# Kernel optimization log

Hardware: AMD Instinct MI355X
Metric: run time of the kernel (lower is better)

## Reference

```python
import jax, jax.numpy as jnp
import numpy as np

NEG_SLOPE = 0.2  # PyG GATConv default leaky_relu slope


def gat_layer(x, src, dst, W, a_src, a_dst, n_nodes, heads, ch):
    # x: [N, in_dim]; W: [in_dim, heads*ch]
    h = (x @ W).reshape(n_nodes, heads, ch)              # [N, H, C]
    e_s = jnp.einsum('nhc,hc->nh', h, a_src)             # [N, H]
    e_d = jnp.einsum('nhc,hc->nh', h, a_dst)             # [N, H]
    e = jax.nn.leaky_relu(e_s[src] + e_d[dst], NEG_SLOPE)  # [E, H]
    # segment softmax over incoming edges of each destination node
    m = jax.lax.stop_gradient(jax.ops.segment_max(e, dst, num_segments=n_nodes))
    w = jnp.exp(e - m[dst])                              # [E, H]
    z = jax.ops.segment_sum(w, dst, num_segments=n_nodes)  # [N, H]
    alpha = w / z[dst]                                   # [E, H]
    msg = h[src] * alpha[:, :, None]                     # [E, H, C]
    out = jax.ops.segment_sum(msg, dst, num_segments=n_nodes)  # [N, H, C]
    return out


def setup_inputs() -> dict:
    key = jax.random.key(0)
    ks = jax.random.split(key, 12)
    N, E, D, H = 50000, 800000, 128, 4
    x = jax.random.normal(ks[0], (N, D), dtype=jnp.float32)
    edge_index = jax.random.randint(ks[1], (2, E), 0, N, dtype=jnp.int64)
    s1 = 1.0 / np.sqrt(D)
    s2 = 1.0 / np.sqrt(D * H)
    W1 = jax.random.normal(ks[2], (D, H * D), dtype=jnp.float32) * s1
    a1_src = jax.random.normal(ks[3], (H, D), dtype=jnp.float32) * s1
    a1_dst = jax.random.normal(ks[4], (H, D), dtype=jnp.float32) * s1
    b1 = jax.random.normal(ks[5], (H * D,), dtype=jnp.float32) * 0.01
    W2 = jax.random.normal(ks[6], (H * D, D), dtype=jnp.float32) * s2
    a2_src = jax.random.normal(ks[7], (1, D), dtype=jnp.float32) * s1
    a2_dst = jax.random.normal(ks[8], (1, D), dtype=jnp.float32) * s1
    b2 = jax.random.normal(ks[9], (D,), dtype=jnp.float32) * 0.01
    fc_w = jax.random.normal(ks[10], (D, 1), dtype=jnp.float32) * s1
    fc_b = jax.random.normal(ks[11], (1,), dtype=jnp.float32) * 0.01
    return {"x": x, "edge_index": edge_index, "W1": W1, "a1_src": a1_src,
            "a1_dst": a1_dst, "b1": b1, "W2": W2, "a2_src": a2_src,
            "a2_dst": a2_dst, "b2": b2, "fc_w": fc_w, "fc_b": fc_b}


def reference(x, edge_index, W1, a1_src, a1_dst, b1, W2, a2_src, a2_dst, b2, fc_w, fc_b):
    N, D = x.shape
    H = a1_src.shape[0]
    # add self-loops (PyG GATConv default add_self_loops=True)
    loop = jnp.arange(N, dtype=edge_index.dtype)
    src = jnp.concatenate([edge_index[0], loop])
    dst = jnp.concatenate([edge_index[1], loop])
    # conv1: heads=4, concat=True -> [N, H*D]
    h1 = gat_layer(x, src, dst, W1, a1_src, a1_dst, N, H, D)
    h1 = jax.nn.relu(h1.reshape(N, H * D) + b1)
    # dropout p=0.2 is identity in eval mode
    # conv2: heads=1 -> [N, D]
    h2 = gat_layer(h1, src, dst, W2, a2_src, a2_dst, N, 1, D)
    h2 = h2.reshape(N, D) + b2
    return h2 @ fc_w + fc_b  # [N, 1]
```

## Files before the change

kernel.cpp:

```cpp
#include <hip/hip_runtime.h>
#include <cstdint>
#include <cstddef>

constexpr int kN   = 50000;
constexpr int kE   = 800000;
constexpr int kEt  = kE + kN;
constexpr float kSlope = 0.2f;
constexpr int kScanB = (kN + 255) / 256;
constexpr int kConvB = (kN * 16 + 255) / 256;
constexpr int kHistB = (kEt + 255) / 256;
constexpr int kQuarB = (kN * 16 + 255) / 256;
constexpr int kHChunks = 64;
constexpr int kChunk   = (kEt + kHChunks - 1) / kHChunks;
constexpr int kHRanges = 4;
constexpr int kRangeN  = kN / kHRanges;
constexpr int kRangeH  = kRangeN / 2;
constexpr int kHalfN   = kN / 2;

typedef __attribute__((ext_vector_type(8))) short bf8_t;
typedef __attribute__((ext_vector_type(4))) float f4_t;
typedef __attribute__((ext_vector_type(2))) float f2_t;

__device__ __align__(16) unsigned short g_xb[(size_t)kN * 128];
__device__ __align__(16) unsigned short g_aggx[(size_t)kN * 512];
__device__ __align__(16) unsigned short g_w1t[4 * 128 * 128];
__device__ __align__(16) float g_u[3][512];
__device__ __align__(16) float g_es1[kN * 4];
__device__ __align__(16) float g_ed1[kN * 4];
__device__ __align__(16) float2 g_sp[kN];
__device__ float g_ed2[kN];
__device__ float g_c0;
__device__ __align__(16) float g_p1s[4 * 128];
__device__ __align__(16) float g_p1d[4 * 128];
__device__ int g_deg[kN];
__device__ int g_ptr[kN + 1];
__device__ int g_rank[kEt];
__device__ __align__(16) unsigned g_bhist[(size_t)kHChunks * kHalfN];
__device__ __align__(16) unsigned g_bbase[(size_t)kHChunks * kHalfN];
__device__ int g_srcs[kEt];
__device__ int g_bsum[kScanB];

__device__ __forceinline__ float lrelu(float x) { return x > 0.f ? x : kSlope * x; }

__device__ __forceinline__ bf8_t bf8_zero() {
  uint4 z = make_uint4(0u, 0u, 0u, 0u);
  return *(bf8_t*)&z;
}

__device__ __forceinline__ unsigned short f2bf1(float v) {
  unsigned u = __float_as_uint(v);
  unsigned r = (u + 0x7FFFu + ((u >> 16) & 1u)) >> 16;
  return (unsigned short)r;
}

__global__ __launch_bounds__(256) void k_hist(const int* __restrict__ ei) {
  __shared__ unsigned sh[kRangeH];
  const int b = blockIdx.x, t = threadIdx.x;
  const int chunk = b & (kHChunks - 1);
  const int rr = b >> 6;
  const int lo = rr * kRangeN, hi = lo + kRangeN;
  for (int i = t; i < kRangeH; i += 256) sh[i] = 0u;
  __syncthreads();
  const int beg = chunk * kChunk, end = min(beg + kChunk, kEt);
  for (int e = beg + t; e < end; e += 256) {
    int d = (e < kE) ? ei[kE + e] : e - kE;
    if (d >= lo && d < hi) {
      unsigned inc = (d & 1) ? 0x10000u : 1u;
      unsigned old = atomicAdd(&sh[(d - lo) >> 1], inc);
      g_rank[e] = (d & 1) ? (int)(old >> 16) : (int)(old & 0xFFFFu);
    }
  }
  __syncthreads();
  unsigned* dst = g_bhist + (size_t)chunk * kHalfN + rr * kRangeH;
  for (int i = t; i < kRangeH; i += 256) dst[i] = sh[i];
}

__global__ __launch_bounds__(256) void k_pass2() {
  const int i = blockIdx.x * 256 + threadIdx.x;
  if (i >= kHalfN) return;
  unsigned c0 = 0, c1 = 0;
#pragma unroll 4
  for (int b = 0; b < kHChunks; ++b) {
    unsigned v = g_bhist[(size_t)b * kHalfN + i];
    g_bbase[(size_t)b * kHalfN + i] = c0 | (c1 << 16);
    c0 += v & 0xFFFFu;
    c1 += v >> 16;
  }
  *(int2*)&g_deg[2 * i] = make_int2((int)c0, (int)c1);
}

__global__ __launch_bounds__(256) void k_init(const float* __restrict__ x,
    const float* __restrict__ W1, const float* __restrict__ W2,
    const float* __restrict__ a1s, const float* __restrict__ a1d,
    const float* __restrict__ a2s, const float* __restrict__ a2d,
    const float* __restrict__ b2, const float* __restrict__ fcw,
    const float* __restrict__ fcb) {
  const int b = blockIdx.x, t = threadIdx.x;
  if (b < 197) {
    int i = b * 256 + t;
    if (i < kN) {
      g_sp[i] = make_float2(0.f, 0.f);
      g_ed2[i] = 0.f;
    }
  } else if (b < 453) {
    int gid = (b - 197) * 256 + t;
    int h = gid >> 14, rem = gid & 16383;
    int c = rem >> 7, j = rem & 127;
    float v = W1[(size_t)c * 512 + h * 128 + j];
    g_w1t[((size_t)h * 128 + j) * 128 + c] = f2bf1(v);
  } else if (b < 457) {
    int gid = (b - 453) * 256 + t;
    int which = gid >> 9, idx = gid & 511;
    int h = idx >> 7, k = idx & 127;
    const float* a = which ? a1d : a1s;
    const float* wrow = W1 + (size_t)k * 512 + h * 128;
    float s = 0.f;
#pragma unroll 8
    for (int c = 0; c < 128; ++c) s += wrow[c] * a[h * 128 + c];
    (which ? g_p1d : g_p1s)[idx] = s;
  } else if (b < 463) {
    int gid = (b - 457) * 256 + t;
    if (gid < 1536) {
      int v = gid >> 9, k = gid & 511;
      const float* vv = v == 0 ? a2s : v == 1 ? a2d : fcw;
      const float* wrow = W2 + (size_t)k * 128;
      float s = 0.f;
#pragma unroll 8
      for (int c = 0; c < 128; ++c) s += wrow[c] * vv[c];
      g_u[v][k] = s;
    }
  } else if (b < 464) {
    if (t < 64) {
      float s = b2[t] * fcw[t] + b2[64 + t] * fcw[64 + t];
#pragma unroll
      for (int off = 32; off > 0; off >>= 1) s += __shfl_down(s, off);
      if (t == 0) g_c0 = s + fcb[0];
    }
  } else {
    int g = (b - 464) * 256 + t;
    if (g < kN * 16) {
      const float* xp = x + (size_t)g * 8;
      float4 f0 = *(const float4*)xp;
      float4 f1 = *(const float4*)(xp + 4);
      unsigned w0 = (unsigned)f2bf1(f0.x) | ((unsigned)f2bf1(f0.y) << 16);
      unsigned w1 = (unsigned)f2bf1(f0.z) | ((unsigned)f2bf1(f0.w) << 16);
      unsigned w2 = (unsigned)f2bf1(f1.x) | ((unsigned)f2bf1(f1.y) << 16);
      unsigned w3 = (unsigned)f2bf1(f1.z) | ((unsigned)f2bf1(f1.w) << 16);
      *(uint4*)(g_xb + (size_t)g * 8) = make_uint4(w0, w1, w2, w3);
    }
  }
}

__device__ __forceinline__ void scores1_body(const float* __restrict__ x,
                                             int bid, int t) {
  const int lane = t & 63;
  const int qt = lane >> 4, ql = lane & 15;
  const int n = ((bid * 256 + t) >> 6) * 4 + qt;
  if (n >= kN) return;
  const float* xp = x + (size_t)n * 128 + ql * 8;
  float4 xa = *(const float4*)xp;
  float4 xb = *(const float4*)(xp + 4);
  float s[4], d[4];
#pragma unroll
  for (int h = 0; h < 4; ++h) {
    const float* ps = g_p1s + h * 128 + ql * 8;
    const float* pd = g_p1d + h * 128 + ql * 8;
    s[h] = xa.x * ps[0] + xa.y * ps[1] + xa.z * ps[2] + xa.w * ps[3]
         + xb.x * ps[4] + xb.y * ps[5] + xb.z * ps[6] + xb.w * ps[7];
    d[h] = xa.x * pd[0] + xa.y * pd[1] + xa.z * pd[2] + xa.w * pd[3]
         + xb.x * pd[4] + xb.y * pd[5] + xb.z * pd[6] + xb.w * pd[7];
  }
#pragma unroll
  for (int off = 1; off < 16; off <<= 1) {
#pragma unroll
    for (int h = 0; h < 4; ++h) {
      s[h] += __shfl_xor(s[h], off);
      d[h] += __shfl_xor(d[h], off);
    }
  }
  if (ql == 0) {
    *(float4*)(g_es1 + (size_t)n * 4) = make_float4(s[0], s[1], s[2], s[3]);
    *(float4*)(g_ed1 + (size_t)n * 4) = make_float4(d[0], d[1], d[2], d[3]);
  }
}

__global__ __launch_bounds__(256) void k_scanA(const float* __restrict__ x) {
  __shared__ int s[256];
  const int b = blockIdx.x, t = threadIdx.x;
  if (b >= kScanB) {
    scores1_body(x, b - kScanB, t);
    return;
  }
  const int i = b * 256 + t;
  int d = (i < kN) ? g_deg[i] : 0;
  s[t] = d;
  __syncthreads();
  for (int off = 1; off < 256; off <<= 1) {
    int v = s[t];
    int u = (t >= off) ? s[t - off] : 0;
    __syncthreads();
    s[t] = v + u;
    __syncthreads();
  }
  if (t == 255) g_bsum[b] = s[255];
  if (i < kN) g_ptr[i] = s[t] - d;
}

__global__ __launch_bounds__(256) void k_scanC() {
  __shared__ int s[256];
  const int b = blockIdx.x, t = threadIdx.x;
  int v = (t < kScanB) ? g_bsum[t] : 0;
  s[t] = v;
  __syncthreads();
  for (int off = 1; off < 256; off <<= 1) {
    int a = s[t];
    int u = (t >= off) ? s[t - off] : 0;
    __syncthreads();
    s[t] = a + u;
    __syncthreads();
  }
  const int boff = (b > 0) ? s[b - 1] : 0;
  __syncthreads();
  const int i = b * 256 + t;
  if (i < kN) g_ptr[i] = g_ptr[i] + boff;
  if (b == 0 && t == 0) g_ptr[kN] = kEt;
}

__global__ __launch_bounds__(256) void k_scatter(const int* __restrict__ ei) {
  int e = blockIdx.x * 256 + threadIdx.x;
  if (e >= kEt) return;
  int s, d;
  if (e < kE) { s = ei[e]; d = ei[kE + e]; } else { s = d = e - kE; }
  const int b = e / kChunk;
  unsigned base = g_bbase[(size_t)b * kHalfN + (d >> 1)];
  base = (d & 1) ? (base >> 16) : (base & 0xFFFFu);
  g_srcs[g_ptr[d] + (int)base + g_rank[e]] = s;
}

__global__ __launch_bounds__(256) void k_agg1x() {
  const int lane = threadIdx.x & 63;
  const int qt = lane >> 4, ql = lane & 15;
  const int n = ((blockIdx.x * 256 + threadIdx.x) >> 6) * 4 + qt;
  if (n >= kN) return;
  const int beg = g_ptr[n], end = g_ptr[n + 1];
  const float4 ed = *(const float4*)(g_ed1 + (size_t)n * 4);
  const int lbase = qt * 16;
  float z0 = 0.f, z1 = 0.f, z2 = 0.f, z3 = 0.f;
  f2_t acc[4][4] = {};
  for (int base = beg; base < end; base += 16) {
    const int cnt = min(16, end - base);
    int s = 0;
    float w0 = 0.f, w1 = 0.f, w2 = 0.f, w3 = 0.f;
    if (ql < cnt) {
      s = g_srcs[base + ql];
      float4 es = *(const float4*)(g_es1 + (size_t)s * 4);
      w0 = __expf(lrelu(es.x + ed.x));
      w1 = __expf(lrelu(es.y + ed.y));
      w2 = __expf(lrelu(es.z + ed.z));
      w3 = __expf(lrelu(es.w + ed.w));
      z0 += w0; z1 += w1; z2 += w2; z3 += w3;
    }
    auto proc = [&](const uint4& uu, int e) {
      float b0 = __shfl(w0, lbase + e), b1 = __shfl(w1, lbase + e);
      float b2 = __shfl(w2, lbase + e), b3 = __shfl(w3, lbase + e);
      f2_t bb0 = b0, bb1 = b1, bb2 = b2, bb3 = b3;
      unsigned ws[4] = {uu.x, uu.y, uu.z, uu.w};
#pragma unroll
      for (int d = 0; d < 4; ++d) {
        f2_t fv;
        fv[0] = __uint_as_float(ws[d] << 16);
        fv[1] = __uint_as_float(ws[d] & 0xFFFF0000u);
        acc[0][d] += bb0 * fv;
        acc[1][d] += bb1 * fv;
        acc[2][d] += bb2 * fv;
        acc[3][d] += bb3 * fv;
      }
    };
    int e = 0;
    for (; e + 4 <= cnt; e += 4) {
      int sj0 = __shfl(s, lbase + e);
      int sj1 = __shfl(s, lbase + e + 1);
      int sj2 = __shfl(s, lbase + e + 2);
      int sj3 = __shfl(s, lbase + e + 3);
      uint4 u0 = *(const uint4*)(g_xb + (size_t)sj0 * 128 + ql * 8);
      uint4 u1 = *(const uint4*)(g_xb + (size_t)sj1 * 128 + ql * 8);
      uint4 u2 = *(const uint4*)(g_xb + (size_t)sj2 * 128 + ql * 8);
      uint4 u3 = *(const uint4*)(g_xb + (size_t)sj3 * 128 + ql * 8);
      proc(u0, e);
      proc(u1, e + 1);
      proc(u2, e + 2);
      proc(u3, e + 3);
    }
    for (; e < cnt; ++e) {
      int sj = __shfl(s, lbase + e);
      uint4 uu = *(const uint4*)(g_xb + (size_t)sj * 128 + ql * 8);
      proc(uu, e);
    }
  }
#pragma unroll
  for (int off = 1; off < 16; off <<= 1) {
    z0 += __shfl_xor(z0, off); z1 += __shfl_xor(z1, off);
    z2 += __shfl_xor(z2, off); z3 += __shfl_xor(z3, off);
  }
  const float iz[4] = {1.f / z0, 1.f / z1, 1.f / z2, 1.f / z3};
  const size_t nb = (size_t)n * 512 + ql * 8;
#pragma unroll
  for (int h = 0; h < 4; ++h) {
    unsigned wd[4];
#pragma unroll
    for (int d = 0; d < 4; ++d) {
      f2_t v = acc[h][d] * iz[h];
      wd[d] = (unsigned)f2bf1(v[0]) | ((unsigned)f2bf1(v[1]) << 16);
    }
    *(uint4*)(g_aggx + nb + h * 128) = make_uint4(wd[0], wd[1], wd[2], wd[3]);
  }
}

__global__ __launch_bounds__(256) void k_fused(const float* __restrict__ b1) {
  __shared__ float sred[2][64][3];
  const int t = threadIdx.x;
  const int lane = t & 63, w = t >> 6;
  const int wrow = w >> 1, wcol = w & 1;
  const int ln15 = lane & 15, q = lane >> 4, qo = q * 8;
  const int row0 = blockIdx.y * 64;
  const int h = blockIdx.z;

  float part[2][4][3] = {};
  f4_t h1acc[2][4] = {};
#pragma unroll
  for (int ks = 0; ks < 128; ks += 32) {
    bf8_t ah[2];
#pragma unroll
    for (int i = 0; i < 2; ++i) {
      int r = row0 + wrow * 32 + i * 16 + ln15;
      ah[i] = bf8_zero();
      if (r < kN)
        ah[i] = *(const bf8_t*)&g_aggx[(size_t)r * 512 + h * 128 + ks + qo];
    }
#pragma unroll
    for (int j = 0; j < 4; ++j) {
      size_t gb = ((size_t)h * 128 + wcol * 64 + j * 16 + ln15) * 128 + ks + qo;
      bf8_t bh = *(const bf8_t*)&g_w1t[gb];
#pragma unroll
      for (int i = 0; i < 2; ++i)
        h1acc[i][j] = __builtin_amdgcn_mfma_f32_16x16x32_bf16(ah[i], bh, h1acc[i][j], 0, 0, 0);
    }
  }
#pragma unroll
  for (int j = 0; j < 4; ++j) {
    int col = h * 128 + wcol * 64 + j * 16 + ln15;
    float bv = b1[col];
    float u0 = g_u[0][col], u1 = g_u[1][col], u2 = g_u[2][col];
#pragma unroll
    for (int i = 0; i < 2; ++i)
#pragma unroll
      for (int reg = 0; reg < 4; ++reg) {
        float v = fmaxf(h1acc[i][j][reg] + bv, 0.f);
        part[i][reg][0] += v * u0;
        part[i][reg][1] += v * u1;
        part[i][reg][2] += v * u2;
      }
  }
#pragma unroll
  for (int off = 1; off < 16; off <<= 1)
#pragma unroll
    for (int i = 0; i < 2; ++i)
#pragma unroll
      for (int reg = 0; reg < 4; ++reg)
#pragma unroll
        for (int v = 0; v < 3; ++v)
          part[i][reg][v] += __shfl_xor(part[i][reg][v], off);
  if (ln15 == 0) {
#pragma unroll
    for (int i = 0; i < 2; ++i)
#pragma unroll
      for (int reg = 0; reg < 4; ++reg) {
        int rl = wrow * 32 + i * 16 + q * 4 + reg;
#pragma unroll
        for (int v = 0; v < 3; ++v) sred[wcol][rl][v] = part[i][reg][v];
      }
  }
  __syncthreads();
  if (t < 192) {
    int row = t / 3, v = t - row * 3;
    float s = sred[0][row][v] + sred[1][row][v];
    int r = row0 + row;
    if (r < kN) {
      float* dst = v == 0 ? &g_sp[r].x : v == 1 ? &g_ed2[r] : &g_sp[r].y;
      atomicAdd(dst, s);
    }
  }
}

__global__ __launch_bounds__(256) void k_agg2s(float* __restrict__ out) {
  const int lane = threadIdx.x & 63;
  const int qt = lane >> 4, ql = lane & 15;
  const int n = ((blockIdx.x * 256 + threadIdx.x) >> 6) * 4 + qt;
  if (n >= kN) return;
  const int beg = g_ptr[n], end = g_ptr[n + 1];
  const float ed = g_ed2[n];
  float zp = 0.f, num = 0.f;
  for (int slot = beg + ql; slot < end; slot += 16) {
    int s = g_srcs[slot];
    float2 sp = g_sp[s];
    float w = __expf(lrelu(sp.x + ed));
    zp += w;
    num += w * sp.y;
  }
#pragma unroll
  for (int off = 1; off < 16; off <<= 1) {
    zp  += __shfl_xor(zp, off);
    num += __shfl_xor(num, off);
  }
  if (ql == 0) out[n] = num / zp + g_c0;
}

extern "C" void kernel_launch(void* const* d_in, const int* in_sizes, int n_in,
                              void* d_out, int out_size, void* d_ws, size_t ws_size,
                              hipStream_t stream) {
  const float* x   = (const float*)d_in[0];
  const int*   ei  = (const int*)d_in[1];
  const float* W1  = (const float*)d_in[2];
  const float* a1s = (const float*)d_in[3];
  const float* a1d = (const float*)d_in[4];
  const float* b1  = (const float*)d_in[5];
  const float* W2  = (const float*)d_in[6];
  const float* a2s = (const float*)d_in[7];
  const float* a2d = (const float*)d_in[8];
  const float* b2  = (const float*)d_in[9];
  const float* fcw = (const float*)d_in[10];
  const float* fcb = (const float*)d_in[11];
  float* out = (float*)d_out;
  (void)d_ws; (void)ws_size; (void)in_sizes; (void)n_in; (void)out_size;

  k_hist<<<kHChunks * kHRanges, 256, 0, stream>>>(ei);
  k_init<<<464 + kConvB, 256, 0, stream>>>(x, W1, W2, a1s, a1d,
                                           a2s, a2d, b2, fcw, fcb);
  k_pass2<<<(kHalfN + 255) / 256, 256, 0, stream>>>();
  k_scanA<<<kScanB + kQuarB, 256, 0, stream>>>(x);
  k_scanC<<<kScanB, 256, 0, stream>>>();
  k_scatter<<<kHistB, 256, 0, stream>>>(ei);

  k_agg1x<<<kQuarB, 256, 0, stream>>>();

  dim3 gf(1, (kN + 63) / 64, 4);
  k_fused<<<gf, 256, 0, stream>>>(b1);

  k_agg2s<<<kQuarB, 256, 0, stream>>>(out);
}
```

Before: 260.6 us.

## Fuse layer-1 aggregation with MFMA projection via shared-memory staging

Merges the layer-1 edge aggregation kernel and the MFMA projection kernel into one kernel. Each block aggregates 32 destination rows into a padded bf16 tile in LDS, then runs the 4-head W1 MFMA and the reductions against the layer-2 vectors directly from LDS. This removes the 50 MB bf16 g_aggx round trip through global memory and one launch. Because each block now owns complete rows, the atomicAdds become plain stores and the zero-initialisation in k_init is dropped. The cost is a 33 KB LDS tile per block, which limits occupancy, a smaller 32-row MFMA tile that reuses each W1 fragment less, and a block-wide barrier between the gather and matmul phases.

Measured after the change: 267.2 us. 1.03x slower.

```diff
diff --git a/kernel.cpp b/kernel.cpp
--- a/kernel.cpp
+++ b/kernel.cpp
@@ -16,13 +16,15 @@
 constexpr int kRangeN  = kN / kHRanges;
 constexpr int kRangeH  = kRangeN / 2;
 constexpr int kHalfN   = kN / 2;
+constexpr int kRows  = 32;
+constexpr int kFB    = (kN + kRows - 1) / kRows;
+constexpr int kPitch = 520;
 
 typedef __attribute__((ext_vector_type(8))) short bf8_t;
 typedef __attribute__((ext_vector_type(4))) float f4_t;
 typedef __attribute__((ext_vector_type(2))) float f2_t;
 
 __device__ __align__(16) unsigned short g_xb[(size_t)kN * 128];
-__device__ __align__(16) unsigned short g_aggx[(size_t)kN * 512];
 __device__ __align__(16) unsigned short g_w1t[4 * 128 * 128];
 __device__ __align__(16) float g_u[3][512];
 __device__ __align__(16) float g_es1[kN * 4];
@@ -42,11 +44,6 @@
 
 __device__ __forceinline__ float lrelu(float x) { return x > 0.f ? x : kSlope * x; }
 
-__device__ __forceinline__ bf8_t bf8_zero() {
-  uint4 z = make_uint4(0u, 0u, 0u, 0u);
-  return *(bf8_t*)&z;
-}
-
 __device__ __forceinline__ unsigned short f2bf1(float v) {
   unsigned u = __float_as_uint(v);
   unsigned r = (u + 0x7FFFu + ((u >> 16) & 1u)) >> 16;
@@ -96,20 +93,14 @@
     const float* __restrict__ b2, const float* __restrict__ fcw,
     const float* __restrict__ fcb) {
   const int b = blockIdx.x, t = threadIdx.x;
-  if (b < 197) {
-    int i = b * 256 + t;
-    if (i < kN) {
-      g_sp[i] = make_float2(0.f, 0.f);
-      g_ed2[i] = 0.f;
-    }
-  } else if (b < 453) {
-    int gid = (b - 197) * 256 + t;
+  if (b < 256) {
+    int gid = b * 256 + t;
     int h = gid >> 14, rem = gid & 16383;
     int c = rem >> 7, j = rem & 127;
     float v = W1[(size_t)c * 512 + h * 128 + j];
     g_w1t[((size_t)h * 128 + j) * 128 + c] = f2bf1(v);
-  } else if (b < 457) {
-    int gid = (b - 453) * 256 + t;
+  } else if (b < 260) {
+    int gid = (b - 256) * 256 + t;
     int which = gid >> 9, idx = gid & 511;
     int h = idx >> 7, k = idx & 127;
     const float* a = which ? a1d : a1s;
@@ -118,8 +109,8 @@
 #pragma unroll 8
     for (int c = 0; c < 128; ++c) s += wrow[c] * a[h * 128 + c];
     (which ? g_p1d : g_p1s)[idx] = s;
-  } else if (b < 463) {
-    int gid = (b - 457) * 256 + t;
+  } else if (b < 266) {
+    int gid = (b - 260) * 256 + t;
     if (gid < 1536) {
       int v = gid >> 9, k = gid & 511;
       const float* vv = v == 0 ? a2s : v == 1 ? a2d : fcw;
@@ -129,7 +120,7 @@
       for (int c = 0; c < 128; ++c) s += wrow[c] * vv[c];
       g_u[v][k] = s;
     }
-  } else if (b < 464) {
+  } else if (b < 267) {
     if (t < 64) {
       float s = b2[t] * fcw[t] + b2[64 + t] * fcw[64 + t];
 #pragma unroll
@@ -137,7 +128,7 @@
       if (t == 0) g_c0 = s + fcb[0];
     }
   } else {
-    int g = (b - 464) * 256 + t;
+    int g = (b - 267) * 256 + t;
     if (g < kN * 16) {
       const float* xp = x + (size_t)g * 8;
       float4 f0 = *(const float4*)xp;
@@ -237,157 +228,153 @@
   g_srcs[g_ptr[d] + (int)base + g_rank[e]] = s;
 }
 
-__global__ __launch_bounds__(256) void k_agg1x() {
-  const int lane = threadIdx.x & 63;
-  const int qt = lane >> 4, ql = lane & 15;
-  const int n = ((blockIdx.x * 256 + threadIdx.x) >> 6) * 4 + qt;
-  if (n >= kN) return;
-  const int beg = g_ptr[n], end = g_ptr[n + 1];
-  const float4 ed = *(const float4*)(g_ed1 + (size_t)n * 4);
-  const int lbase = qt * 16;
-  float z0 = 0.f, z1 = 0.f, z2 = 0.f, z3 = 0.f;
-  f2_t acc[4][4] = {};
-  for (int base = beg; base < end; base += 16) {
-    const int cnt = min(16, end - base);
-    int s = 0;
-    float w0 = 0.f, w1 = 0.f, w2 = 0.f, w3 = 0.f;
-    if (ql < cnt) {
-      s = g_srcs[base + ql];
-      float4 es = *(const float4*)(g_es1 + (size_t)s * 4);
-      w0 = __expf(lrelu(es.x + ed.x));
-      w1 = __expf(lrelu(es.y + ed.y));
-      w2 = __expf(lrelu(es.z + ed.z));
-      w3 = __expf(lrelu(es.w + ed.w));
-      z0 += w0; z1 += w1; z2 += w2; z3 += w3;
-    }
-    auto proc = [&](const uint4& uu, int e) {
-      float b0 = __shfl(w0, lbase + e), b1 = __shfl(w1, lbase + e);
-      float b2 = __shfl(w2, lbase + e), b3 = __shfl(w3, lbase + e);
-      f2_t bb0 = b0, bb1 = b1, bb2 = b2, bb3 = b3;
-      unsigned ws[4] = {uu.x, uu.y, uu.z, uu.w};
-#pragma unroll
-      for (int d = 0; d < 4; ++d) {
-        f2_t fv;
-        fv[0] = __uint_as_float(ws[d] << 16);
-        fv[1] = __uint_as_float(ws[d] & 0xFFFF0000u);
-        acc[0][d] += bb0 * fv;
-        acc[1][d] += bb1 * fv;
-        acc[2][d] += bb2 * fv;
-        acc[3][d] += bb3 * fv;
-      }
-    };
-    int e = 0;
-    for (; e + 4 <= cnt; e += 4) {
-      int sj0 = __shfl(s, lbase + e);
-      int sj1 = __shfl(s, lbase + e + 1);
-      int sj2 = __shfl(s, lbase + e + 2);
-      int sj3 = __shfl(s, lbase + e + 3);
-      uint4 u0 = *(const uint4*)(g_xb + (size_t)sj0 * 128 + ql * 8);
-      uint4 u1 = *(const uint4*)(g_xb + (size_t)sj1 * 128 + ql * 8);
-      uint4 u2 = *(const uint4*)(g_xb + (size_t)sj2 * 128 + ql * 8);
-      uint4 u3 = *(const uint4*)(g_xb + (size_t)sj3 * 128 + ql * 8);
-      proc(u0, e);
-      proc(u1, e + 1);
-      proc(u2, e + 2);
-      proc(u3, e + 3);
-    }
-    for (; e < cnt; ++e) {
-      int sj = __shfl(s, lbase + e);
-      uint4 uu = *(const uint4*)(g_xb + (size_t)sj * 128 + ql * 8);
-      proc(uu, e);
-    }
-  }
-#pragma unroll
-  for (int off = 1; off < 16; off <<= 1) {
-    z0 += __shfl_xor(z0, off); z1 += __shfl_xor(z1, off);
-    z2 += __shfl_xor(z2, off); z3 += __shfl_xor(z3, off);
-  }
-  const float iz[4] = {1.f / z0, 1.f / z1, 1.f / z2, 1.f / z3};
-  const size_t nb = (size_t)n * 512 + ql * 8;
-#pragma unroll
-  for (int h = 0; h < 4; ++h) {
-    unsigned wd[4];
-#pragma unroll
-    for (int d = 0; d < 4; ++d) {
-      f2_t v = acc[h][d] * iz[h];
-      wd[d] = (unsigned)f2bf1(v[0]) | ((unsigned)f2bf1(v[1]) << 16);
-    }
-    *(uint4*)(g_aggx + nb + h * 128) = make_uint4(wd[0], wd[1], wd[2], wd[3]);
-  }
-}
-
-__global__ __launch_bounds__(256) void k_fused(const float* __restrict__ b1) {
-  __shared__ float sred[2][64][3];
+__global__ __launch_bounds__(256, 4) void k_fagg(const float* __restrict__ b1) {
+  __shared__ unsigned short sm[kRows * kPitch];
+  __shared__ float sred[2][kRows][3];
   const int t = threadIdx.x;
   const int lane = t & 63, w = t >> 6;
+  const int qt = lane >> 4, ql = lane & 15;
+  const int row0 = blockIdx.x * kRows;
+  const int lbase = qt * 16;
+
+  for (int pass = 0; pass < 2; ++pass) {
+    const int nn = pass * 16 + w * 4 + qt;
+    const int n = row0 + nn;
+    int beg = 0, end = 0;
+    float4 ed = make_float4(0.f, 0.f, 0.f, 0.f);
+    if (n < kN) {
+      beg = g_ptr[n];
+      end = g_ptr[n + 1];
+      ed = *(const float4*)(g_ed1 + (size_t)n * 4);
+    }
+    float z0 = 0.f, z1 = 0.f, z2 = 0.f, z3 = 0.f;
+    f2_t acc[4][4] = {};
+    for (int base = beg; base < end; base += 16) {
+      const int cnt = min(16, end - base);
+      int s = 0;
+      float w0 = 0.f, w1 = 0.f, w2 = 0.f, w3 = 0.f;
+      if (ql < cnt) {
+        s = g_srcs[base + ql];
+        float4 es = *(const float4*)(g_es1 + (size_t)s * 4);
+        w0 = __expf(lrelu(es.x + ed.x));
+        w1 = __expf(lrelu(es.y + ed.y));
+        w2 = __expf(lrelu(es.z + ed.z));
+        w3 = __expf(lrelu(es.w + ed.w));
+        z0 += w0; z1 += w1; z2 += w2; z3 += w3;
+      }
+      auto proc = [&](const uint4& uu, int e) {
+        float b0 = __shfl(w0, lbase + e), b1v = __shfl(w1, lbase + e);
+        float b2 = __shfl(w2, lbase + e), b3 = __shfl(w3, lbase + e);
+        f2_t bb0 = b0, bb1 = b1v, bb2 = b2, bb3 = b3;
+        unsigned ws[4] = {uu.x, uu.y, uu.z, uu.w};
+#pragma unroll
+        for (int d = 0; d < 4; ++d) {
+          f2_t fv;
+          fv[0] = __uint_as_float(ws[d] << 16);
+          fv[1] = __uint_as_float(ws[d] & 0xFFFF0000u);
+          acc[0][d] += bb0 * fv;
+          acc[1][d] += bb1 * fv;
+          acc[2][d] += bb2 * fv;
+          acc[3][d] += bb3 * fv;
+        }
+      };
+      int e = 0;
+      for (; e + 4 <= cnt; e += 4) {
+        int sj0 = __shfl(s, lbase + e);
+        int sj1 = __shfl(s, lbase + e + 1);
+        int sj2 = __shfl(s, lbase + e + 2);
+        int sj3 = __shfl(s, lbase + e + 3);
+        uint4 u0 = *(const uint4*)(g_xb + (size_t)sj0 * 128 + ql * 8);
+        uint4 u1 = *(const uint4*)(g_xb + (size_t)sj1 * 128 + ql * 8);
+        uint4 u2 = *(const uint4*)(g_xb + (size_t)sj2 * 128 + ql * 8);
+        uint4 u3 = *(const uint4*)(g_xb + (size_t)sj3 * 128 + ql * 8);
+        proc(u0, e);
+        proc(u1, e + 1);
+        proc(u2, e + 2);
+        proc(u3, e + 3);
+      }
+      for (; e < cnt; ++e) {
+        int sj = __shfl(s, lbase + e);
+        uint4 uu = *(const uint4*)(g_xb + (size_t)sj * 128 + ql * 8);
+        proc(uu, e);
+      }
+    }
+#pragma unroll
+    for (int off = 1; off < 16; off <<= 1) {
+      z0 += __shfl_xor(z0, off); z1 += __shfl_xor(z1, off);
+      z2 += __shfl_xor(z2, off); z3 += __shfl_xor(z3, off);
+    }
+    const bool valid = end > beg;
+    const float izz[4] = {valid ? 1.f / z0 : 0.f, valid ? 1.f / z1 : 0.f,
+                          valid ? 1.f / z2 : 0.f, valid ? 1.f / z3 : 0.f};
+    const int sb = nn * kPitch + ql * 8;
+#pragma unroll
+    for (int h = 0; h < 4; ++h) {
+      unsigned wd[4];
+#pragma unroll
+      for (int d = 0; d < 4; ++d) {
+        f2_t v = acc[h][d] * izz[h];
+        wd[d] = (unsigned)f2bf1(v[0]) | ((unsigned)f2bf1(v[1]) << 16);
+      }
+      *(uint4*)&sm[sb + h * 128] = make_uint4(wd[0], wd[1], wd[2], wd[3]);
+    }
+  }
+  __syncthreads();
+
   const int wrow = w >> 1, wcol = w & 1;
-  const int ln15 = lane & 15, q = lane >> 4, qo = q * 8;
-  const int row0 = blockIdx.y * 64;
-  const int h = blockIdx.z;
-
-  float part[2][4][3] = {};
-  f4_t h1acc[2][4] = {};
-#pragma unroll
-  for (int ks = 0; ks < 128; ks += 32) {
-    bf8_t ah[2];
-#pragma unroll
-    for (int i = 0; i < 2; ++i) {
-      int r = row0 + wrow * 32 + i * 16 + ln15;
-      ah[i] = bf8_zero();
-      if (r < kN)
-        ah[i] = *(const bf8_t*)&g_aggx[(size_t)r * 512 + h * 128 + ks + qo];
+  const int qo = qt * 8;
+  float part[4][3] = {};
+#pragma unroll
+  for (int h = 0; h < 4; ++h) {
+    f4_t h1acc[4] = {};
+#pragma unroll
+    for (int ks = 0; ks < 128; ks += 32) {
+      bf8_t ah = *(const bf8_t*)&sm[(wrow * 16 + ql) * kPitch + h * 128 + ks + qo];
+#pragma unroll
+      for (int j = 0; j < 4; ++j) {
+        size_t gb = ((size_t)h * 128 + wcol * 64 + j * 16 + ql) * 128 + ks + qo;
+        bf8_t bh = *(const bf8_t*)&g_w1t[gb];
+        h1acc[j] = __builtin_amdgcn_mfma_f32_16x16x32_bf16(ah, bh, h1acc[j], 0, 0, 0);
+      }
     }
 #pragma unroll
     for (int j = 0; j < 4; ++j) {
-      size_t gb = ((size_t)h * 128 + wcol * 64 + j * 16 + ln15) * 128 + ks + qo;
-      bf8_t bh = *(const bf8_t*)&g_w1t[gb];
-#pragma unroll
-      for (int i = 0; i < 2; ++i)
-        h1acc[i][j] = __builtin_amdgcn_mfma_f32_16x16x32_bf16(ah[i], bh, h1acc[i][j], 0, 0, 0);
-    }
-  }
-#pragma unroll
-  for (int j = 0; j < 4; ++j) {
-    int col = h * 128 + wcol * 64 + j * 16 + ln15;
-    float bv = b1[col];
-    float u0 = g_u[0][col], u1 = g_u[1][col], u2 = g_u[2][col];
-#pragma unroll
-    for (int i = 0; i < 2; ++i)
+      int col = h * 128 + wcol * 64 + j * 16 + ql;
+      float bv = b1[col];
+      float u0 = g_u[0][col], u1 = g_u[1][col], u2 = g_u[2][col];
 #pragma unroll
       for (int reg = 0; reg < 4; ++reg) {
-        float v = fmaxf(h1acc[i][j][reg] + bv, 0.f);
-        part[i][reg][0] += v * u0;
-        part[i][reg][1] += v * u1;
-        part[i][reg][2] += v * u2;
-      }
+        float v = fmaxf(h1acc[j][reg] + bv, 0.f);
+        part[reg][0] += v * u0;
+        part[reg][1] += v * u1;
+        part[reg][2] += v * u2;
+      }
+    }
   }
 #pragma unroll
   for (int off = 1; off < 16; off <<= 1)
 #pragma unroll
-    for (int i = 0; i < 2; ++i)
-#pragma unroll
-      for (int reg = 0; reg < 4; ++reg)
-#pragma unroll
-        for (int v = 0; v < 3; ++v)
-          part[i][reg][v] += __shfl_xor(part[i][reg][v], off);
-  if (ln15 == 0) {
-#pragma unroll
-    for (int i = 0; i < 2; ++i)
-#pragma unroll
-      for (int reg = 0; reg < 4; ++reg) {
-        int rl = wrow * 32 + i * 16 + q * 4 + reg;
-#pragma unroll
-        for (int v = 0; v < 3; ++v) sred[wcol][rl][v] = part[i][reg][v];
-      }
-  }
-  __syncthreads();
-  if (t < 192) {
+    for (int reg = 0; reg < 4; ++reg)
+#pragma unroll
+      for (int v = 0; v < 3; ++v)
+        part[reg][v] += __shfl_xor(part[reg][v], off);
+  if (ql == 0) {
+#pragma unroll
+    for (int reg = 0; reg < 4; ++reg) {
+      int rl = wrow * 16 + qt * 4 + reg;
+#pragma unroll
+      for (int v = 0; v < 3; ++v) sred[wcol][rl][v] = part[reg][v];
+    }
+  }
+  __syncthreads();
+  if (t < 96) {
     int row = t / 3, v = t - row * 3;
-    float s = sred[0][row][v] + sred[1][row][v];
+    float sv = sred[0][row][v] + sred[1][row][v];
     int r = row0 + row;
     if (r < kN) {
-      float* dst = v == 0 ? &g_sp[r].x : v == 1 ? &g_ed2[r] : &g_sp[r].y;
-      atomicAdd(dst, s);
+      if (v == 0)      g_sp[r].x = sv;
+      else if (v == 1) g_ed2[r]  = sv;
+      else             g_sp[r].y = sv;
     }
   }
 }
@@ -434,17 +421,14 @@
   (void)d_ws; (void)ws_size; (void)in_sizes; (void)n_in; (void)out_size;
 
   k_hist<<<kHChunks * kHRanges, 256, 0, stream>>>(ei);
-  k_init<<<464 + kConvB, 256, 0, stream>>>(x, W1, W2, a1s, a1d,
+  k_init<<<267 + kConvB, 256, 0, stream>>>(x, W1, W2, a1s, a1d,
                                            a2s, a2d, b2, fcw, fcb);
   k_pass2<<<(kHalfN + 255) / 256, 256, 0, stream>>>();
   k_scanA<<<kScanB + kQuarB, 256, 0, stream>>>(x);
   k_scanC<<<kScanB, 256, 0, stream>>>();
   k_scatter<<<kHistB, 256, 0, stream>>>(ei);
 
-  k_agg1x<<<kQuarB, 256, 0, stream>>>();
-
-  dim3 gf(1, (kN + 63) / 64, 4);
-  k_fused<<<gf, 256, 0, stream>>>(b1);
+  k_fagg<<<kFB, 256, 0, stream>>>(b1);
 
   k_agg2s<<<kQuarB, 256, 0, stream>>>(out);
 }
```
